# Kernel tuning notes

Measured on AMD Instinct MI355X. Metric: run time of the kernel, lower is better.

The kernel has to match this reference:

```python
import jax, jax.numpy as jnp
import numpy as np

POS_KL_W = 0.1
NEG_KL_W = 0.02
ORDER_W = 0.5
N_BINS = 1000
SIGMA = 0.1
EPS = 1e-09


def setup_inputs() -> dict:
    key = jax.random.key(0)
    k1, k2, k3 = jax.random.split(key, 3)
    N, D, C = 256, 512, 16
    T_F = jax.random.normal(k1, (N, D), dtype=jnp.float32)
    S_F = jax.random.normal(k2, (N, D), dtype=jnp.float32)
    labels = jax.random.uniform(k3, (N, C), dtype=jnp.float32)  # argmax -> class ids
    return {"T_F": T_F, "S_F": S_F, "labels": labels}


def _histograms_and_means(x, pos_labels, neg_labels, t):
    # x: [N, D]; L2-normalize rows (eps matches F.normalize default 1e-12)
    norm = jnp.maximum(jnp.linalg.norm(x, axis=-1, keepdims=True), 1e-12)
    xn = x / norm
    cos = xn @ xn.T                      # [N, N]
    dists = cos.reshape(-1)              # [N*N]
    # Gaussian soft-binning: [N*N, N_BINS] (the big memory-bound intermediate)
    delta = jnp.exp(-0.5 * ((dists[:, None] - t[None, :]) / SIGMA) ** 2)
    neg_w = neg_labels.reshape(-1)
    pos_w = pos_labels.reshape(-1)
    neg_p = (neg_w @ delta) / jnp.sum(neg_w)   # [N_BINS]
    pos_p = (pos_w @ delta) / jnp.sum(pos_w)   # [N_BINS]
    E_pos = jnp.sum(cos * pos_labels, axis=-1) / jnp.sum(pos_labels, axis=-1)  # [N]
    E_neg = jnp.sum(cos * neg_labels, axis=-1) / jnp.sum(neg_labels, axis=-1)  # [N]
    return neg_p, pos_p, E_neg, E_pos


def _kl(anchor, dist):
    # torch F.kl_div(log(dist+eps), anchor+eps, reduction='batchmean'); batch dim is 1
    a = anchor + EPS
    d = dist + EPS
    return jnp.sum(a * (jnp.log(a) - jnp.log(d)))


def reference(T_F, S_F, labels):
    N = T_F.shape[0]
    t = jnp.arange(-1.0, 1.0, 2.0 / N_BINS, dtype=jnp.float32)  # [1000] bin centers
    lab = jnp.argmax(labels, axis=-1)                            # [N]
    grid = (lab[None, :] == lab[:, None]).astype(jnp.float32)    # [N, N]
    neg_labels = 1.0 - grid
    pos_labels = grid * (1.0 - jnp.eye(N, dtype=jnp.float32))

    neg_t, pos_t, E_neg_t, E_pos_t = _histograms_and_means(T_F, pos_labels, neg_labels, t)
    neg_s, pos_s, E_neg_s, E_pos_s = _histograms_and_means(S_F, pos_labels, neg_labels, t)

    pos_kl = POS_KL_W * _kl(pos_t, pos_s)
    neg_kl = NEG_KL_W * _kl(neg_t, neg_s)
    o1 = jnp.mean(jnp.abs(E_pos_t - E_pos_s))
    o2 = jnp.mean(jnp.abs(E_neg_t - E_neg_s))
    o3 = jnp.mean(E_pos_s - E_neg_s)
    order_loss = ORDER_W * (o1 + o2 + o3)
    return pos_kl + neg_kl + order_loss
```

## Files before the change

### kernel.cpp

```cpp
#include <hip/hip_runtime.h>
#include <math.h>

#define N 256
#define D 512
#define C 16
#define NBINS 1000
#define MCELL 1000
#define MSTRIDE 1024
#define EPSF 1e-9f
#define KEXP2 -72.134752f
#define TAILB 64

__device__ inline float waveReduceSum(float v) {
#pragma unroll
    for (int off = 32; off > 0; off >>= 1) v += __shfl_down(v, off, 64);
    return v;
}
__device__ inline double waveReduceSumD(double v) {
#pragma unroll
    for (int off = 32; off > 0; off >>= 1) v += __shfl_down(v, off, 64);
    return v;
}

__global__ void k_prep(const float* __restrict__ labels, int* __restrict__ lab,
                       float* __restrict__ mg, unsigned int* __restrict__ cnt) {
    int b = blockIdx.x;
    int tid = threadIdx.x;
    if (b < 12) {
        ((float4*)mg)[b * 256 + tid] = make_float4(0.f, 0.f, 0.f, 0.f);
    } else {
        if (tid == 0) cnt[0] = 0u;
        float best = labels[tid * C];
        int bi = 0;
#pragma unroll
        for (int c = 1; c < C; ++c) {
            float v = labels[tid * C + c];
            if (v > best) { best = v; bi = c; }
        }
        lab[tid] = bi;
    }
}

__global__ void __launch_bounds__(512) k_main(
        const float* __restrict__ T, const float* __restrict__ S,
        const int* __restrict__ lab, float* __restrict__ mg,
        float* __restrict__ Earr, float* __restrict__ cpos) {
    int mat = blockIdx.y;
    int i0 = blockIdx.x * 4;
    int t = threadIdx.x;
    int h = t >> 8, jj = t & 255;
    const float* X = mat ? S : T;

    __shared__ float rows[4 * D];
    __shared__ float psum[5][512];
    __shared__ float invs[256];
    __shared__ float mom[6 * MSTRIDE];
    __shared__ float red[8][6];

    for (int i = t; i < 6 * MSTRIDE; i += 512) mom[i] = 0.f;
#pragma unroll
    for (int f = t; f < 4 * D; f += 512) rows[f] = X[i0 * D + f];
    __syncthreads();

    float d0 = 0.f, d1 = 0.f, d2 = 0.f, d3 = 0.f, ssq = 0.f;
    {
        const float4* xrow = (const float4*)(X + (size_t)jj * D + h * 256);
        const float4* r0 = (const float4*)(rows + 0 * D + h * 256);
        const float4* r1 = (const float4*)(rows + 1 * D + h * 256);
        const float4* r2 = (const float4*)(rows + 2 * D + h * 256);
        const float4* r3 = (const float4*)(rows + 3 * D + h * 256);
#pragma unroll 8
        for (int k4 = 0; k4 < 64; ++k4) {
            float4 xj = xrow[k4];
            float4 a = r0[k4];
            float4 b = r1[k4];
            float4 c = r2[k4];
            float4 e = r3[k4];
            d0 = fmaf(a.x, xj.x, fmaf(a.y, xj.y, fmaf(a.z, xj.z, fmaf(a.w, xj.w, d0))));
            d1 = fmaf(b.x, xj.x, fmaf(b.y, xj.y, fmaf(b.z, xj.z, fmaf(b.w, xj.w, d1))));
            d2 = fmaf(c.x, xj.x, fmaf(c.y, xj.y, fmaf(c.z, xj.z, fmaf(c.w, xj.w, d2))));
            d3 = fmaf(e.x, xj.x, fmaf(e.y, xj.y, fmaf(e.z, xj.z, fmaf(e.w, xj.w, d3))));
            ssq = fmaf(xj.x, xj.x, fmaf(xj.y, xj.y, fmaf(xj.z, xj.z, fmaf(xj.w, xj.w, ssq))));
        }
    }
    psum[0][t] = d0; psum[1][t] = d1; psum[2][t] = d2; psum[3][t] = d3;
    psum[4][t] = ssq;
    __syncthreads();
    if (t < 256) {
        float sq = psum[4][t] + psum[4][t + 256];
        invs[t] = 1.0f / fmaxf(sqrtf(sq), 1e-12f);
    }
    __syncthreads();

    float invj = invs[jj];
    float av[4];
#pragma unroll
    for (int r = 0; r < 4; ++r)
        av[r] = (psum[r][jj] + psum[r][jj + 256]) * invs[i0 + r] * invj;

    int labj = lab[jj];
    float wp[4];
#pragma unroll
    for (int r = 0; r < 4; ++r)
        wp[r] = (labj == lab[i0 + r] && jj != i0 + r) ? 1.f : 0.f;

#pragma unroll
    for (int rr = 0; rr < 2; ++rr) {
        int r = h * 2 + rr;
        if (jj != i0 + r) {
            float d = av[r];
            int jc = (int)floorf((d + 1.f) * 500.f);
            jc = max(0, min(jc, MCELL - 1));
            float del = d - (-1.f + ((float)jc + 0.5f) * 0.002f);
            float dd = del * del;
            atomicAdd(&mom[jc], 1.f);
            atomicAdd(&mom[MSTRIDE + jc], del);
            atomicAdd(&mom[2 * MSTRIDE + jc], dd);
            if (wp[r] > 0.f) {
                atomicAdd(&mom[3 * MSTRIDE + jc], 1.f);
                atomicAdd(&mom[4 * MSTRIDE + jc], del);
                atomicAdd(&mom[5 * MSTRIDE + jc], dd);
            }
        }
    }

    {
        int rA = h * 2, rB = h * 2 + 1;
        float r0v = waveReduceSum((jj != i0 + rA) ? av[rA] : 0.f);
        float r1v = waveReduceSum(av[rA] * wp[rA]);
        float r2v = waveReduceSum(wp[rA]);
        float r3v = waveReduceSum((jj != i0 + rB) ? av[rB] : 0.f);
        float r4v = waveReduceSum(av[rB] * wp[rB]);
        float r5v = waveReduceSum(wp[rB]);
        int wid = t >> 6, lane = t & 63;
        if (lane == 0) {
            red[wid][0] = r0v; red[wid][1] = r1v; red[wid][2] = r2v;
            red[wid][3] = r3v; red[wid][4] = r4v; red[wid][5] = r5v;
        }
    }
    __syncthreads();
    if (t < 4) {
        int wb = (t >> 1) * 4;
        int sel = (t & 1) * 3;
        float sA = 0, sP = 0, cP = 0;
        for (int w = 0; w < 4; ++w) {
            sA += red[wb + w][sel + 0];
            sP += red[wb + w][sel + 1];
            cP += red[wb + w][sel + 2];
        }
        int row = i0 + t;
        Earr[(mat * 2 + 0) * N + row] = sP / cP;
        Earr[(mat * 2 + 1) * N + row] = (sA - sP) / (255.f - cP);
        if (mat == 0) cpos[row] = cP;
    }
    for (int i = t; i < 6 * MSTRIDE; i += 512) {
        float v = mom[i];
        if (v != 0.f) atomicAdd(&mg[mat * 6144 + i], v);
    }
}

__global__ void __launch_bounds__(256) k_tail(const float* __restrict__ mg,
                                              const float* __restrict__ Earr,
                                              const float* __restrict__ cpos,
                                              float* __restrict__ pkl,
                                              unsigned int* __restrict__ cnt,
                                              float* __restrict__ out) {
    int b = blockIdx.x;
    int tid = threadIdx.x;
    int wid = tid >> 6, lane = tid & 63;
    __shared__ float sm[12288];
    __shared__ float binres[16][4];
    __shared__ float kterm[16][2];
    __shared__ float credL[4];
    __shared__ unsigned int old_s;
    __shared__ double dred[4][5];

    for (int i = tid; i < 3072; i += 256)
        ((float4*)sm)[i] = ((const float4*)mg)[i];

    float cv = cpos[tid];
    cv = waveReduceSum(cv);
    if (lane == 0) credL[wid] = cv;
    __syncthreads();
    float pcnt = credL[0] + credL[1] + credL[2] + credL[3];
    float ncnt = 65280.f - pcnt;

    int u = tid >> 4, sub = tid & 15;
    int bin = b * 16 + u;
    float t = -1.f + 0.002f * (float)bin;
    float paT = 0.f, saT = 0.f, paS = 0.f, saS = 0.f;
    for (int c = sub; c < MCELL; c += 16) {
        float m0T = sm[c], m0S = sm[6144 + c];
        if (m0T == 0.f && m0S == 0.f) continue;
        float cj = -1.f + ((float)c + 0.5f) * 0.002f;
        float q = cj - t;
        float q2 = q * q;
        if (q2 < 0.5f) {
            float E = __builtin_amdgcn_exp2f(KEXP2 * q2);
            float u1 = 100.f * q;
            float w2 = fmaf(0.5f * u1, u1, -50.f);
            saT = fmaf(E, fmaf(w2, sm[2048 + c], fmaf(-u1, sm[1024 + c], m0T)), saT);
            paT = fmaf(E, fmaf(w2, sm[5120 + c], fmaf(-u1, sm[4096 + c], sm[3072 + c])), paT);
            saS = fmaf(E, fmaf(w2, sm[6144 + 2048 + c], fmaf(-u1, sm[6144 + 1024 + c], m0S)), saS);
            paS = fmaf(E, fmaf(w2, sm[6144 + 5120 + c], fmaf(-u1, sm[6144 + 4096 + c], sm[6144 + 3072 + c])), paS);
        }
    }
#pragma unroll
    for (int off = 1; off < 16; off <<= 1) {
        paT += __shfl_xor(paT, off, 16);
        saT += __shfl_xor(saT, off, 16);
        paS += __shfl_xor(paS, off, 16);
        saS += __shfl_xor(saS, off, 16);
    }
    if (sub == 0) {
        binres[u][0] = paT; binres[u][1] = saT;
        binres[u][2] = paS; binres[u][3] = saS;
    }
    __syncthreads();

    if (tid < 16) {
        int bn = b * 16 + tid;
        float pk = 0.f, nk = 0.f;
        if (bn < NBINS) {
            float hpT = binres[tid][0], hsT = binres[tid][1];
            float hpS = binres[tid][2], hsS = binres[tid][3];
            float pt = hpT / pcnt;
            float nt = (hsT - hpT) / ncnt;
            float ps = hpS / pcnt;
            float ns = (hsS - hpS) / ncnt;
            pk = (pt + EPSF) * (__logf(pt + EPSF) - __logf(ps + EPSF));
            nk = (nt + EPSF) * (__logf(nt + EPSF) - __logf(ns + EPSF));
        }
        kterm[tid][0] = pk;
        kterm[tid][1] = nk;
    }
    __syncthreads();
    if (tid == 0) {
        float a = 0.f, bb = 0.f;
        for (int q = 0; q < 16; ++q) { a += kterm[q][0]; bb += kterm[q][1]; }
        pkl[b * 2] = a;
        pkl[b * 2 + 1] = bb;
        __threadfence();
        old_s = atomicAdd(cnt, 1u);
    }
    __syncthreads();
    if (old_s != TAILB - 1) return;

    __threadfence();
    double a = 0.0, bb = 0.0;
    if (tid < TAILB) {
        volatile const float* vp = pkl;
        a = (double)vp[2 * tid];
        bb = (double)vp[2 * tid + 1];
    }
    a = waveReduceSumD(a);
    bb = waveReduceSumD(bb);
    double o1, o2, o3;
    {
        float ept = Earr[0 * N + tid];
        float ent = Earr[1 * N + tid];
        float eps_ = Earr[2 * N + tid];
        float ens = Earr[3 * N + tid];
        o1 = fabs((double)ept - (double)eps_);
        o2 = fabs((double)ent - (double)ens);
        o3 = (double)eps_ - (double)ens;
    }
    o1 = waveReduceSumD(o1);
    o2 = waveReduceSumD(o2);
    o3 = waveReduceSumD(o3);
    if (lane == 0) {
        dred[wid][0] = a;  dred[wid][1] = bb;
        dred[wid][2] = o1; dred[wid][3] = o2; dred[wid][4] = o3;
    }
    __syncthreads();
    if (tid == 0) {
        double A = dred[0][0], B = dred[0][1];
        double Co = 0, Do = 0, Eo = 0;
        for (int w = 0; w < 4; ++w) {
            Co += dred[w][2]; Do += dred[w][3]; Eo += dred[w][4];
        }
        double loss = 0.1 * A + 0.02 * B + 0.5 * ((Co + Do + Eo) / (double)N);
        out[0] = (float)loss;
    }
}

extern "C" void kernel_launch(void* const* d_in, const int* in_sizes, int n_in,
                              void* d_out, int out_size, void* d_ws, size_t ws_size,
                              hipStream_t stream) {
    const float* T = (const float*)d_in[0];
    const float* S = (const float*)d_in[1];
    const float* labels = (const float*)d_in[2];
    float* out = (float*)d_out;

    float* ws = (float*)d_ws;
    float* mg = ws;
    float* Earr = mg + 12288;
    float* cpos = Earr + 1024;
    float* pkl = cpos + 256;
    unsigned int* cnt = (unsigned int*)(pkl + 128);
    int* lab = (int*)(cnt + 1);

    k_prep<<<13, 256, 0, stream>>>(labels, lab, mg, cnt);
    k_main<<<dim3(N / 4, 2), 512, 0, stream>>>(T, S, lab, mg, Earr, cpos);
    k_tail<<<TAILB, 256, 0, stream>>>(mg, Earr, cpos, pkl, cnt, out);
}
```

Before: 48.13 us.

## Fuse prep, main and tail into one persistent kernel with grid barriers

```diff
diff --git a/kernel.cpp b/kernel.cpp
--- a/kernel.cpp
+++ b/kernel.cpp
@@ -9,7 +9,8 @@
 #define MSTRIDE 1024
 #define EPSF 1e-9f
 #define KEXP2 -72.134752f
-#define TAILB 64
+#define NBLK 128
+#define NTAIL 64
 
 __device__ inline float waveReduceSum(float v) {
 #pragma unroll
@@ -22,43 +23,41 @@
     return v;
 }
 
-__global__ void k_prep(const float* __restrict__ labels, int* __restrict__ lab,
-                       float* __restrict__ mg, unsigned int* __restrict__ cnt) {
-    int b = blockIdx.x;
-    int tid = threadIdx.x;
-    if (b < 12) {
-        ((float4*)mg)[b * 256 + tid] = make_float4(0.f, 0.f, 0.f, 0.f);
-    } else {
-        if (tid == 0) cnt[0] = 0u;
-        float best = labels[tid * C];
-        int bi = 0;
-#pragma unroll
-        for (int c = 1; c < C; ++c) {
-            float v = labels[tid * C + c];
-            if (v > best) { best = v; bi = c; }
-        }
-        lab[tid] = bi;
-    }
-}
-
-__global__ void __launch_bounds__(512) k_main(
+__global__ void __launch_bounds__(512) k_mega(
         const float* __restrict__ T, const float* __restrict__ S,
-        const int* __restrict__ lab, float* __restrict__ mg,
-        float* __restrict__ Earr, float* __restrict__ cpos) {
-    int mat = blockIdx.y;
-    int i0 = blockIdx.x * 4;
+        const float* __restrict__ labels,
+        float* __restrict__ partial, float* __restrict__ mg,
+        float* __restrict__ Earr, float* __restrict__ cpos,
+        float* __restrict__ hbp, float* __restrict__ hbs,
+        unsigned int* __restrict__ cnt, float* __restrict__ out) {
+    int bid = blockIdx.x;
+    int mat = bid >> 6;
+    int i0 = (bid & 63) << 2;
     int t = threadIdx.x;
     int h = t >> 8, jj = t & 255;
+    int wid = t >> 6, lane = t & 63;
     const float* X = mat ? S : T;
 
     __shared__ float rows[4 * D];
     __shared__ float psum[5][512];
     __shared__ float invs[256];
+    __shared__ int   labs[256];
     __shared__ float mom[6 * MSTRIDE];
     __shared__ float red[8][6];
-
+    __shared__ float pcnt_s;
+    __shared__ double dred[8][5];
+
+    if (t < 256) {
+        float best = labels[t * C];
+        int bi = 0;
+#pragma unroll
+        for (int c = 1; c < C; ++c) {
+            float v = labels[t * C + c];
+            if (v > best) { best = v; bi = c; }
+        }
+        labs[t] = bi;
+    }
     for (int i = t; i < 6 * MSTRIDE; i += 512) mom[i] = 0.f;
-#pragma unroll
     for (int f = t; f < 4 * D; f += 512) rows[f] = X[i0 * D + f];
     __syncthreads();
 
@@ -98,11 +97,11 @@
     for (int r = 0; r < 4; ++r)
         av[r] = (psum[r][jj] + psum[r][jj + 256]) * invs[i0 + r] * invj;
 
-    int labj = lab[jj];
+    int labj = labs[jj];
     float wp[4];
 #pragma unroll
     for (int r = 0; r < 4; ++r)
-        wp[r] = (labj == lab[i0 + r] && jj != i0 + r) ? 1.f : 0.f;
+        wp[r] = (labj == labs[i0 + r] && jj != i0 + r) ? 1.f : 0.f;
 
 #pragma unroll
     for (int rr = 0; rr < 2; ++rr) {
@@ -123,7 +122,6 @@
             }
         }
     }
-
     {
         int rA = h * 2, rB = h * 2 + 1;
         float r0v = waveReduceSum((jj != i0 + rA) ? av[rA] : 0.f);
@@ -132,7 +130,6 @@
         float r3v = waveReduceSum((jj != i0 + rB) ? av[rB] : 0.f);
         float r4v = waveReduceSum(av[rB] * wp[rB]);
         float r5v = waveReduceSum(wp[rB]);
-        int wid = t >> 6, lane = t & 63;
         if (lane == 0) {
             red[wid][0] = r0v; red[wid][1] = r1v; red[wid][2] = r2v;
             red[wid][3] = r3v; red[wid][4] = r4v; red[wid][5] = r5v;
@@ -140,8 +137,7 @@
     }
     __syncthreads();
     if (t < 4) {
-        int wb = (t >> 1) * 4;
-        int sel = (t & 1) * 3;
+        int wb = (t >> 1) * 4, sel = (t & 1) * 3;
         float sA = 0, sP = 0, cP = 0;
         for (int w = 0; w < 4; ++w) {
             sA += red[wb + w][sel + 0];
@@ -153,130 +149,143 @@
         Earr[(mat * 2 + 1) * N + row] = (sA - sP) / (255.f - cP);
         if (mat == 0) cpos[row] = cP;
     }
-    for (int i = t; i < 6 * MSTRIDE; i += 512) {
-        float v = mom[i];
-        if (v != 0.f) atomicAdd(&mg[mat * 6144 + i], v);
-    }
-}
-
-__global__ void __launch_bounds__(256) k_tail(const float* __restrict__ mg,
-                                              const float* __restrict__ Earr,
-                                              const float* __restrict__ cpos,
-                                              float* __restrict__ pkl,
-                                              unsigned int* __restrict__ cnt,
-                                              float* __restrict__ out) {
-    int b = blockIdx.x;
-    int tid = threadIdx.x;
-    int wid = tid >> 6, lane = tid & 63;
-    __shared__ float sm[12288];
-    __shared__ float binres[16][4];
-    __shared__ float kterm[16][2];
-    __shared__ float credL[4];
-    __shared__ unsigned int old_s;
-    __shared__ double dred[4][5];
-
-    for (int i = tid; i < 3072; i += 256)
-        ((float4*)sm)[i] = ((const float4*)mg)[i];
-
-    float cv = cpos[tid];
-    cv = waveReduceSum(cv);
-    if (lane == 0) credL[wid] = cv;
-    __syncthreads();
-    float pcnt = credL[0] + credL[1] + credL[2] + credL[3];
-    float ncnt = 65280.f - pcnt;
-
-    int u = tid >> 4, sub = tid & 15;
-    int bin = b * 16 + u;
-    float t = -1.f + 0.002f * (float)bin;
-    float paT = 0.f, saT = 0.f, paS = 0.f, saS = 0.f;
-    for (int c = sub; c < MCELL; c += 16) {
-        float m0T = sm[c], m0S = sm[6144 + c];
-        if (m0T == 0.f && m0S == 0.f) continue;
-        float cj = -1.f + ((float)c + 0.5f) * 0.002f;
-        float q = cj - t;
+    {
+        float4* dst = (float4*)(partial + (size_t)bid * 6144);
+        const float4* src = (const float4*)mom;
+        for (int i = t; i < 1536; i += 512) dst[i] = src[i];
+    }
+    __syncthreads();
+    if (t == 0) {
+        __threadfence();
+        atomicAdd(&cnt[0], 1u);
+    }
+    if (bid >= NTAIL) return;
+
+    if (t == 0) {
+        while (__hip_atomic_load(&cnt[0], __ATOMIC_ACQUIRE,
+                                 __HIP_MEMORY_SCOPE_AGENT) < NBLK) {
+            __builtin_amdgcn_s_sleep(1);
+        }
+    }
+    __syncthreads();
+
+    if (t < 192) {
+        int o = bid * 192 + t;
+        int mo = (o >= 6144) ? 1 : 0;
+        int c = o - mo * 6144;
+        const float* src = partial + (size_t)(mo << 6) * 6144 + c;
+        float acc = 0.f;
+#pragma unroll 8
+        for (int p = 0; p < 64; ++p) acc += src[(size_t)p * 6144];
+        mg[o] = acc;
+    }
+    __syncthreads();
+    if (t == 0) {
+        __threadfence();
+        atomicAdd(&cnt[1], 1u);
+        while (__hip_atomic_load(&cnt[1], __ATOMIC_ACQUIRE,
+                                 __HIP_MEMORY_SCOPE_AGENT) < NTAIL) {
+            __builtin_amdgcn_s_sleep(1);
+        }
+    }
+    __syncthreads();
+
+    int mat3 = bid >> 5;
+    int bslot = bid & 31;
+    {
+        const float4* src = (const float4*)(mg + mat3 * 6144);
+        float4* dst = (float4*)mom;
+        for (int i = t; i < 1536; i += 512) dst[i] = src[i];
+    }
+    if (t < 256) {
+        float cv = cpos[t];
+        cv = waveReduceSum(cv);
+        if (lane == 0) red[wid][0] = cv;
+    }
+    __syncthreads();
+    if (t == 0) pcnt_s = red[0][0] + red[1][0] + red[2][0] + red[3][0];
+    __syncthreads();
+
+    int u = t >> 4, sub = t & 15;
+    int bin = bslot * 32 + u;
+    float tb = -1.f + 0.002f * (float)bin;
+    float pa = 0.f, sa = 0.f;
+    for (int cc = sub; cc < MCELL; cc += 16) {
+        float m0 = mom[cc];
+        if (m0 == 0.f) continue;
+        float cj = -1.f + ((float)cc + 0.5f) * 0.002f;
+        float q = cj - tb;
         float q2 = q * q;
         if (q2 < 0.5f) {
             float E = __builtin_amdgcn_exp2f(KEXP2 * q2);
             float u1 = 100.f * q;
             float w2 = fmaf(0.5f * u1, u1, -50.f);
-            saT = fmaf(E, fmaf(w2, sm[2048 + c], fmaf(-u1, sm[1024 + c], m0T)), saT);
-            paT = fmaf(E, fmaf(w2, sm[5120 + c], fmaf(-u1, sm[4096 + c], sm[3072 + c])), paT);
-            saS = fmaf(E, fmaf(w2, sm[6144 + 2048 + c], fmaf(-u1, sm[6144 + 1024 + c], m0S)), saS);
-            paS = fmaf(E, fmaf(w2, sm[6144 + 5120 + c], fmaf(-u1, sm[6144 + 4096 + c], sm[6144 + 3072 + c])), paS);
+            sa = fmaf(E, fmaf(w2, mom[2048 + cc], fmaf(-u1, mom[1024 + cc], m0)), sa);
+            pa = fmaf(E, fmaf(w2, mom[5120 + cc], fmaf(-u1, mom[4096 + cc], mom[3072 + cc])), pa);
         }
     }
 #pragma unroll
     for (int off = 1; off < 16; off <<= 1) {
-        paT += __shfl_xor(paT, off, 16);
-        saT += __shfl_xor(saT, off, 16);
-        paS += __shfl_xor(paS, off, 16);
-        saS += __shfl_xor(saS, off, 16);
-    }
-    if (sub == 0) {
-        binres[u][0] = paT; binres[u][1] = saT;
-        binres[u][2] = paS; binres[u][3] = saS;
-    }
-    __syncthreads();
-
-    if (tid < 16) {
-        int bn = b * 16 + tid;
-        float pk = 0.f, nk = 0.f;
+        pa += __shfl_xor(pa, off, 16);
+        sa += __shfl_xor(sa, off, 16);
+    }
+    if (sub == 0 && bin < NBINS) {
+        hbp[mat3 * NBINS + bin] = pa;
+        hbs[mat3 * NBINS + bin] = sa;
+    }
+    __syncthreads();
+    unsigned int old = 0u;
+    if (t == 0) {
+        __threadfence();
+        old = atomicAdd(&cnt[2], 1u);
+        red[0][0] = (float)old;
+    }
+    __syncthreads();
+    if ((unsigned int)red[0][0] != NTAIL - 1) return;
+
+    __threadfence();
+    float pcnt = pcnt_s;
+    float ncnt = 65280.f - pcnt;
+    volatile const float* vhp = hbp;
+    volatile const float* vhs = hbs;
+    double poskl = 0, negkl = 0, o1 = 0, o2 = 0, o3 = 0;
+#pragma unroll
+    for (int it = 0; it < 2; ++it) {
+        int bn = t + it * 512;
         if (bn < NBINS) {
-            float hpT = binres[tid][0], hsT = binres[tid][1];
-            float hpS = binres[tid][2], hsS = binres[tid][3];
+            float hpT = vhp[bn], hsT = vhs[bn];
+            float hpS = vhp[NBINS + bn], hsS = vhs[NBINS + bn];
             float pt = hpT / pcnt;
             float nt = (hsT - hpT) / ncnt;
             float ps = hpS / pcnt;
             float ns = (hsS - hpS) / ncnt;
-            pk = (pt + EPSF) * (__logf(pt + EPSF) - __logf(ps + EPSF));
-            nk = (nt + EPSF) * (__logf(nt + EPSF) - __logf(ns + EPSF));
-        }
-        kterm[tid][0] = pk;
-        kterm[tid][1] = nk;
-    }
-    __syncthreads();
-    if (tid == 0) {
-        float a = 0.f, bb = 0.f;
-        for (int q = 0; q < 16; ++q) { a += kterm[q][0]; bb += kterm[q][1]; }
-        pkl[b * 2] = a;
-        pkl[b * 2 + 1] = bb;
-        __threadfence();
-        old_s = atomicAdd(cnt, 1u);
-    }
-    __syncthreads();
-    if (old_s != TAILB - 1) return;
-
-    __threadfence();
-    double a = 0.0, bb = 0.0;
-    if (tid < TAILB) {
-        volatile const float* vp = pkl;
-        a = (double)vp[2 * tid];
-        bb = (double)vp[2 * tid + 1];
-    }
-    a = waveReduceSumD(a);
-    bb = waveReduceSumD(bb);
-    double o1, o2, o3;
-    {
-        float ept = Earr[0 * N + tid];
-        float ent = Earr[1 * N + tid];
-        float eps_ = Earr[2 * N + tid];
-        float ens = Earr[3 * N + tid];
+            poskl += (double)((pt + EPSF) * (__logf(pt + EPSF) - __logf(ps + EPSF)));
+            negkl += (double)((nt + EPSF) * (__logf(nt + EPSF) - __logf(ns + EPSF)));
+        }
+    }
+    if (t < N) {
+        float ept = Earr[0 * N + t];
+        float ent = Earr[1 * N + t];
+        float eps_ = Earr[2 * N + t];
+        float ens = Earr[3 * N + t];
         o1 = fabs((double)ept - (double)eps_);
         o2 = fabs((double)ent - (double)ens);
         o3 = (double)eps_ - (double)ens;
     }
+    poskl = waveReduceSumD(poskl);
+    negkl = waveReduceSumD(negkl);
     o1 = waveReduceSumD(o1);
     o2 = waveReduceSumD(o2);
     o3 = waveReduceSumD(o3);
     if (lane == 0) {
-        dred[wid][0] = a;  dred[wid][1] = bb;
+        dred[wid][0] = poskl; dred[wid][1] = negkl;
         dred[wid][2] = o1; dred[wid][3] = o2; dred[wid][4] = o3;
     }
     __syncthreads();
-    if (tid == 0) {
-        double A = dred[0][0], B = dred[0][1];
-        double Co = 0, Do = 0, Eo = 0;
-        for (int w = 0; w < 4; ++w) {
+    if (t == 0) {
+        double A = 0, B = 0, Co = 0, Do = 0, Eo = 0;
+        for (int w = 0; w < 8; ++w) {
+            A += dred[w][0]; B += dred[w][1];
             Co += dred[w][2]; Do += dred[w][3]; Eo += dred[w][4];
         }
         double loss = 0.1 * A + 0.02 * B + 0.5 * ((Co + Do + Eo) / (double)N);
@@ -293,14 +302,15 @@
     float* out = (float*)d_out;
 
     float* ws = (float*)d_ws;
-    float* mg = ws;
+    float* partial = ws;
+    float* mg = partial + (size_t)NBLK * 6144;
     float* Earr = mg + 12288;
     float* cpos = Earr + 1024;
-    float* pkl = cpos + 256;
-    unsigned int* cnt = (unsigned int*)(pkl + 128);
-    int* lab = (int*)(cnt + 1);
-
-    k_prep<<<13, 256, 0, stream>>>(labels, lab, mg, cnt);
-    k_main<<<dim3(N / 4, 2), 512, 0, stream>>>(T, S, lab, mg, Earr, cpos);
-    k_tail<<<TAILB, 256, 0, stream>>>(mg, Earr, cpos, pkl, cnt, out);
+    float* hbp = cpos + 256;
+    float* hbs = hbp + 2 * NBINS;
+    unsigned int* cnt = (unsigned int*)(hbs + 2 * NBINS);
+
+    hipMemsetAsync(cnt, 0, 3 * sizeof(unsigned int), stream);
+    k_mega<<<NBLK, 512, 0, stream>>>(T, S, labels, partial, mg, Earr, cpos,
+                                     hbp, hbs, cnt, out);
 }
```

After: 62.38 us. 29.6% more time.
